# Kernel optimization log

Hardware: AMD Instinct MI355X
Metric: run time of the kernel (lower is better)

## Reference

```python
import jax, jax.numpy as jnp
import numpy as np

N_NODES = 50000
N_EDGES = 800000
D_IN = 128
D_OUT = 128


def setup_inputs() -> dict:
    key = jax.random.key(0)
    ks = jax.random.split(key, 10)
    x = jax.random.normal(ks[0], (N_NODES, D_IN), dtype=jnp.float32)
    src = jax.random.randint(ks[1], (N_EDGES,), 0, N_NODES, dtype=jnp.int32)
    dst = jax.random.randint(ks[2], (N_EDGES,), 0, N_NODES, dtype=jnp.int32)
    s = 1.0 / np.sqrt(D_IN)
    def lin(k, din, dout):
        kw, kb = jax.random.split(k)
        W = jax.random.uniform(kw, (din, dout), minval=-s, maxval=s, dtype=jnp.float32)
        b = jax.random.uniform(kb, (dout,), minval=-s, maxval=s, dtype=jnp.float32)
        return W, b
    W1, b1 = lin(ks[3], D_IN, D_IN)
    W2, b2 = lin(ks[4], D_IN, D_IN)
    W3, b3 = lin(ks[5], D_IN, D_OUT)
    return dict(x=x, W1=W1, b1=b1, W2=W2, b2=b2, W3=W3, b3=b3, src=src, dst=dst)


def reference(x, W1, b1, W2, b2, W3, b3, src, dst):
    n = x.shape[0]
    ones = jnp.ones(src.shape[0], dtype=x.dtype)
    in_deg = jax.ops.segment_sum(ones, dst, num_segments=n)    # [N]
    out_deg = jax.ops.segment_sum(ones, src, num_segments=n)   # [N]

    def sage_gcn(h, W, b):
        # DGL SAGEConv(aggregator_type='gcn'), eval mode (feat_drop = identity):
        # h_neigh = (sum_{j in N(i)} h_j + h_i) / (in_deg_i + 1); out = h_neigh @ W + b
        neigh = jax.ops.segment_sum(h[src], dst, num_segments=n)  # [N, D]
        h_neigh = (neigh + h) / (in_deg + 1.0)[:, None]
        return h_neigh @ W + b

    h = sage_gcn(x, W1, b1)
    h = sage_gcn(h, W2, b2)

    # DGL GraphConv norm='both', allow_zero_in_degree=True:
    # out = D_in^{-1/2} A D_out^{-1/2} h W + b, degrees clamped to >= 1
    norm_out = jnp.clip(out_deg, 1.0) ** -0.5
    norm_in = jnp.clip(in_deg, 1.0) ** -0.5
    hs = h * norm_out[:, None]
    agg = jax.ops.segment_sum(hs[src], dst, num_segments=n)
    out = (agg * norm_in[:, None]) @ W3 + b3
    return out
```

## Files before the change

### kernel.cpp

```cpp
#include <hip/hip_runtime.h>

#define NN 50000
#define NE 800000
#define D 128

#define CH 64
#define EPC (NE / CH)
#define RG 8
#define NPR (NN / RG)

typedef short bf16x8 __attribute__((ext_vector_type(8)));
typedef float f32x4 __attribute__((ext_vector_type(4)));


__device__ __forceinline__ unsigned bf16rne(float f) {
  unsigned u = __float_as_uint(f);
  return (u + 0x7fffu + ((u >> 16) & 1u)) >> 16;
}
__device__ __forceinline__ unsigned packbf(float lo, float hi) {
  return bf16rne(lo) | (bf16rne(hi) << 16);
}

__global__ __launch_bounds__(256) void cvtw_kernel(const float* __restrict__ x,
                                                   const float* __restrict__ W1,
                                                   const float* __restrict__ W2,
                                                   const float* __restrict__ W3,
                                                   unsigned short* __restrict__ hbf,
                                                   unsigned short* __restrict__ tbl2,
                                                   unsigned short* __restrict__ T1,
                                                   unsigned short* __restrict__ T2,
                                                   unsigned short* __restrict__ T3) {
  int b = blockIdx.x;
  int tid = threadIdx.x;
  if (b < 6250) {
    int i = b * 256 + tid;
    float4 v = ((const float4*)x)[i];
    uint2 p;
    p.x = packbf(v.x, v.y);
    p.y = packbf(v.z, v.w);
    ((uint2*)hbf)[i] = p;
  } else if (b < 6442) {
    int g = b - 6250;
    int w = g >> 6;
    int i = (g & 63) * 256 + tid;
    const float* W = (w == 0) ? W1 : (w == 1) ? W2 : W3;
    unsigned short* T = (w == 0) ? T1 : (w == 1) ? T2 : T3;
    int n = i >> 7, k = i & 127;
    T[n * 128 + k] = (unsigned short)bf16rne(W[k * 128 + n]);
  } else {
    if (tid < 16) {
      ((uint4*)(hbf + (size_t)NN * D))[tid] = make_uint4(0, 0, 0, 0);
      ((uint4*)(tbl2 + (size_t)NN * D))[tid] = make_uint4(0, 0, 0, 0);
    }
  }
}

__global__ __launch_bounds__(1024) void hist_kernel(const int* __restrict__ src,
                                                    const int* __restrict__ dst,
                                                    int* __restrict__ partial_dst,
                                                    int* __restrict__ partial_src) {
  __shared__ int hd[NPR];
  __shared__ int hs[NPR];
  int tid = threadIdx.x;
  int c = blockIdx.x >> 3;
  int r = blockIdx.x & 7;
  int base = r * NPR;
  for (int i = tid; i < NPR; i += 1024) { hd[i] = 0; hs[i] = 0; }
  __syncthreads();
  int e0 = c * EPC;
  for (int i = tid; i < EPC; i += 1024) {
    int d = dst[e0 + i];
    int s = src[e0 + i];
    unsigned dr = (unsigned)(d - base);
    unsigned sr = (unsigned)(s - base);
    if (dr < NPR) atomicAdd(&hd[dr], 1);
    if (sr < NPR) atomicAdd(&hs[sr], 1);
  }
  __syncthreads();
  for (int i = tid; i < NPR; i += 1024) {
    partial_dst[c * NN + base + i] = hd[i];
    partial_src[c * NN + base + i] = hs[i];
  }
}

__device__ __forceinline__ int block_excl_scan(int v, int* wsum) {
  int lane = threadIdx.x & 63;
  int w = threadIdx.x >> 6;
  int incl = v;
#pragma unroll
  for (int off = 1; off < 64; off <<= 1) {
    int t = __shfl_up(incl, off);
    if (lane >= off) incl += t;
  }
  if (lane == 63) wsum[w] = incl;
  __syncthreads();
  int wo = 0;
#pragma unroll
  for (int j = 0; j < 4; ++j)
    if (j < w) wo += wsum[j];
  return wo + incl - v;
}

__global__ __launch_bounds__(256) void degscan_kernel(int* __restrict__ partial_dst,
                                                      const int* __restrict__ partial_src,
                                                      int* __restrict__ degtmp,
                                                      int* __restrict__ deg_out,
                                                      int* __restrict__ row_ptr,
                                                      int* __restrict__ partials, int N) {
  __shared__ int wsum[4];
  int d = blockIdx.x * 256 + threadIdx.x;
  int run = 0;
  if (d < N) {
#pragma unroll
    for (int c = 0; c < CH; ++c) {
      int v = partial_dst[c * NN + d];
      partial_dst[c * NN + d] = run;
      run += v;
    }
    degtmp[d] = run;
    int ro = 0;
#pragma unroll
    for (int c = 0; c < CH; ++c) ro += partial_src[c * NN + d];
    deg_out[d] = ro;
  }
  int pad = (run + 15) & ~15;
  int excl = block_excl_scan(pad, wsum);
  if (d < N) row_ptr[d] = excl;
  if (threadIdx.x == 255) partials[blockIdx.x] = excl + pad;
}

__global__ __launch_bounds__(256) void scan2(int* __restrict__ partials,
                                             int* __restrict__ row_ptr, int nb, int N) {
  __shared__ int wsum[4];
  int v = (threadIdx.x < nb) ? partials[threadIdx.x] : 0;
  int excl = block_excl_scan(v, wsum);
  if (threadIdx.x < nb) partials[threadIdx.x] = excl;
  if (threadIdx.x == nb - 1) row_ptr[N] = excl + v;
}

__global__ __launch_bounds__(256) void scan3(int* __restrict__ row_ptr,
                                             const int* __restrict__ partials, int N) {
  int i = blockIdx.x * 256 + threadIdx.x;
  if (i < N) row_ptr[i] += partials[blockIdx.x];
}

__global__ __launch_bounds__(1024) void fill_kernel(const int* __restrict__ src,
                                                    const int* __restrict__ dst,
                                                    const int* __restrict__ row_ptr,
                                                    const int* __restrict__ partial_dst,
                                                    const int* __restrict__ degtmp,
                                                    int* __restrict__ csr_src) {
  __shared__ int cur[NPR];
  int tid = threadIdx.x;
  int c = blockIdx.x >> 3;
  int r = blockIdx.x & 7;
  int base = r * NPR;
  for (int i = tid; i < NPR; i += 1024)
    cur[i] = row_ptr[base + i] + partial_dst[c * NN + base + i];
  if (c == 0) {
    for (int i = tid; i < NPR; i += 1024) {
      int node = base + i;
      int s = row_ptr[node] + degtmp[node];
      int e = row_ptr[node + 1];
      for (int j = s; j < e; ++j) csr_src[j] = NN;
    }
  }
  __syncthreads();
  int e0 = c * EPC;
  for (int i = tid; i < EPC; i += 1024) {
    int d = dst[e0 + i];
    unsigned dr = (unsigned)(d - base);
    if (dr < NPR) {
      int pos = atomicAdd(&cur[dr], 1);
      csr_src[pos] = src[e0 + i];
    }
  }
}

__device__ __forceinline__ void bacc(float* a, uint4 u) {
  a[0] += __uint_as_float(u.x << 16);
  a[1] += __uint_as_float(u.x & 0xffff0000u);
  a[2] += __uint_as_float(u.y << 16);
  a[3] += __uint_as_float(u.y & 0xffff0000u);
  a[4] += __uint_as_float(u.z << 16);
  a[5] += __uint_as_float(u.z & 0xffff0000u);
  a[6] += __uint_as_float(u.w << 16);
  a[7] += __uint_as_float(u.w & 0xffff0000u);
}

template <int AMODE, int GMODE, int OUT_BF>
__global__ __launch_bounds__(256, 4) void fused_kernel(
    const unsigned short* __restrict__ hb, const int* __restrict__ row_ptr,
    const int* __restrict__ csr_src, const int* __restrict__ degtmp,
    const int* __restrict__ deg_out, const unsigned short* __restrict__ WT,
    const float* __restrict__ bias, float* __restrict__ outf,
    unsigned short* __restrict__ outb, int N) {
  __shared__ unsigned short sA[4][16 * 136];
  int tid = threadIdx.x;
  int wv = tid >> 6;
  int lane = tid & 63;
  int q = lane >> 4;
  int col = lane & 15;
  int base = blockIdx.x * 64 + wv * 16;

  for (int j = 0; j < 16; ++j) {
    int node = base + j;
    int cn = (node < N) ? node : N - 1;
    int start = row_ptr[cn];
    int iters = (row_ptr[cn + 1] - start) >> 4;
    float a0[8] = {0, 0, 0, 0, 0, 0, 0, 0};
    float a1[8] = {0, 0, 0, 0, 0, 0, 0, 0};
    float a2[8] = {0, 0, 0, 0, 0, 0, 0, 0};
    float a3[8] = {0, 0, 0, 0, 0, 0, 0, 0};
    const int* ce = csr_src + start + q;
    for (int it = 0; it < iters; ++it, ce += 16) {
      int i0 = ce[0];
      int i1 = ce[4];
      int i2 = ce[8];
      int i3 = ce[12];
      uint4 u0 = ((const uint4*)(hb + (size_t)i0 * D))[col];
      uint4 u1 = ((const uint4*)(hb + (size_t)i1 * D))[col];
      uint4 u2 = ((const uint4*)(hb + (size_t)i2 * D))[col];
      uint4 u3 = ((const uint4*)(hb + (size_t)i3 * D))[col];
      bacc(a0, u0);
      bacc(a1, u1);
      bacc(a2, u2);
      bacc(a3, u3);
    }
#pragma unroll
    for (int t = 0; t < 8; ++t) a0[t] = (a0[t] + a1[t]) + (a2[t] + a3[t]);
#pragma unroll
    for (int t = 0; t < 8; ++t) {
      a0[t] += __shfl_xor(a0[t], 16);
      a0[t] += __shfl_xor(a0[t], 32);
    }
    int indeg = degtmp[cn];
    if (AMODE == 0) {
      uint4 s = ((const uint4*)(hb + (size_t)cn * D))[col];
      float sf[8] = {0, 0, 0, 0, 0, 0, 0, 0};
      bacc(sf, s);
      float inv = 1.0f / (float)(indeg + 1);
#pragma unroll
      for (int t = 0; t < 8; ++t) a0[t] = (a0[t] + sf[t]) * inv;
    } else {
      float sc = rsqrtf(fmaxf((float)indeg, 1.0f));
#pragma unroll
      for (int t = 0; t < 8; ++t) a0[t] *= sc;
    }
    if (q == 0) {
      uint4 p;
      p.x = packbf(a0[0], a0[1]);
      p.y = packbf(a0[2], a0[3]);
      p.z = packbf(a0[4], a0[5]);
      p.w = packbf(a0[6], a0[7]);
      *(uint4*)&sA[wv][j * 136 + col * 8] = p;
    }
  }

  int ln = col;
  bf16x8 af[4];
#pragma unroll
  for (int c = 0; c < 4; ++c)
    af[c] = *(const bf16x8*)&sA[wv][ln * 136 + c * 32 + q * 8];
  f32x4 acc[8];
#pragma unroll
  for (int t = 0; t < 8; ++t) acc[t] = (f32x4){0.f, 0.f, 0.f, 0.f};
#pragma unroll
  for (int t = 0; t < 8; ++t) {
    const unsigned short* Wr = WT + (size_t)(t * 16 + ln) * 128 + q * 8;
    bf16x8 b0 = *(const bf16x8*)(Wr + 0);
    bf16x8 b1 = *(const bf16x8*)(Wr + 32);
    bf16x8 b2 = *(const bf16x8*)(Wr + 64);
    bf16x8 b3 = *(const bf16x8*)(Wr + 96);
    acc[t] = __builtin_amdgcn_mfma_f32_16x16x32_bf16(af[0], b0, acc[t], 0, 0, 0);
    acc[t] = __builtin_amdgcn_mfma_f32_16x16x32_bf16(af[1], b1, acc[t], 0, 0, 0);
    acc[t] = __builtin_amdgcn_mfma_f32_16x16x32_bf16(af[2], b2, acc[t], 0, 0, 0);
    acc[t] = __builtin_amdgcn_mfma_f32_16x16x32_bf16(af[3], b3, acc[t], 0, 0, 0);
  }
  float scl[4];
#pragma unroll
  for (int r = 0; r < 4; ++r) {
    scl[r] = 1.0f;
    if (GMODE == 1) {
      int row = base + q * 4 + r;
      int rr = (row < N) ? row : 0;
      scl[r] = rsqrtf(fmaxf((float)deg_out[rr], 1.0f));
    }
  }
#pragma unroll
  for (int t = 0; t < 8; ++t) {
    float b = bias[t * 16 + ln];
#pragma unroll
    for (int r = 0; r < 4; ++r) {
      int row = base + q * 4 + r;
      if (row < N) {
        float v = (acc[t][r] + b) * scl[r];
        if (OUT_BF)
          outb[(size_t)row * 128 + t * 16 + ln] = (unsigned short)bf16rne(v);
        else
          outf[(size_t)row * 128 + t * 16 + ln] = v;
      }
    }
  }
}


extern "C" void kernel_launch(void* const* d_in, const int* in_sizes, int n_in,
                              void* d_out, int out_size, void* d_ws, size_t ws_size,
                              hipStream_t stream) {
  const float* x = (const float*)d_in[0];
  const float* W1 = (const float*)d_in[1];
  const float* b1 = (const float*)d_in[2];
  const float* W2 = (const float*)d_in[3];
  const float* b2 = (const float*)d_in[4];
  const float* W3 = (const float*)d_in[5];
  const float* b3 = (const float*)d_in[6];
  const int* src = (const int*)d_in[7];
  const int* dst = (const int*)d_in[8];
  float* out = (float*)d_out;

  const int N = NN;

  unsigned short* hbf = (unsigned short*)d_ws;
  unsigned short* tbl2 = hbf + (size_t)(NN + 1) * D;
  unsigned short* WT1 = tbl2 + (size_t)(NN + 1) * D;
  unsigned short* WT2 = WT1 + D * D;
  unsigned short* WT3 = WT2 + D * D;
  int* partial_dst = (int*)(WT3 + D * D);
  int* partial_src = partial_dst + (size_t)CH * NN;
  int* degtmp = partial_src + (size_t)CH * NN;
  int* deg_out = degtmp + NN;
  int* row_ptr = deg_out + NN;
  int* partials = row_ptr + NN + 1;
  int* csr_src = partials + 256;

  const int scanBlocks = (N + 255) / 256;

  cvtw_kernel<<<6443, 256, 0, stream>>>(x, W1, W2, W3, hbf, tbl2, WT1, WT2, WT3);
  hist_kernel<<<CH * RG, 1024, 0, stream>>>(src, dst, partial_dst, partial_src);
  degscan_kernel<<<scanBlocks, 256, 0, stream>>>(partial_dst, partial_src, degtmp,
                                                 deg_out, row_ptr, partials, N);
  scan2<<<1, 256, 0, stream>>>(partials, row_ptr, scanBlocks, N);
  scan3<<<scanBlocks, 256, 0, stream>>>(row_ptr, partials, N);
  fill_kernel<<<CH * RG, 1024, 0, stream>>>(src, dst, row_ptr, partial_dst, degtmp, csr_src);

  int fusedBlocks = (N + 63) / 64;

  fused_kernel<0, 0, 1><<<fusedBlocks, 256, 0, stream>>>(
      hbf, row_ptr, csr_src, degtmp, deg_out, WT1, b1, nullptr, tbl2, N);
  fused_kernel<0, 1, 1><<<fusedBlocks, 256, 0, stream>>>(
      tbl2, row_ptr, csr_src, degtmp, deg_out, WT2, b2, nullptr, hbf, N);
  fused_kernel<1, 0, 0><<<fusedBlocks, 256, 0, stream>>>(
      hbf, row_ptr, csr_src, degtmp, deg_out, WT3, b3, out, nullptr, N);
}
```

Measured before the change: 317.0 us.

## Shrink fused blocks to 16 nodes and split MFMA output columns across waves

Each block now handles 16 nodes instead of 64. Each wave aggregates 4 nodes into one shared tile, then after a block barrier computes 2 of the 8 output column tiles. This gives 4x more blocks, which should help load balance across CUs for the irregular gather. It also cuts the per-wave MFMA accumulator count, and the N bounds checks are dropped on the assumption that N is a multiple of 16. The cost is an added __syncthreads and removal of the min-blocks-per-CU launch bound hint.

```diff
diff --git a/kernel.cpp b/kernel.cpp
--- a/kernel.cpp
+++ b/kernel.cpp
@@ -189,25 +189,26 @@
 }
 
 template <int AMODE, int GMODE, int OUT_BF>
-__global__ __launch_bounds__(256, 4) void fused_kernel(
+__global__ __launch_bounds__(256) void fused_kernel(
     const unsigned short* __restrict__ hb, const int* __restrict__ row_ptr,
     const int* __restrict__ csr_src, const int* __restrict__ degtmp,
     const int* __restrict__ deg_out, const unsigned short* __restrict__ WT,
     const float* __restrict__ bias, float* __restrict__ outf,
     unsigned short* __restrict__ outb, int N) {
-  __shared__ unsigned short sA[4][16 * 136];
+  __shared__ unsigned short sA[16 * 136];
   int tid = threadIdx.x;
   int wv = tid >> 6;
   int lane = tid & 63;
   int q = lane >> 4;
   int col = lane & 15;
-  int base = blockIdx.x * 64 + wv * 16;
-
-  for (int j = 0; j < 16; ++j) {
-    int node = base + j;
-    int cn = (node < N) ? node : N - 1;
-    int start = row_ptr[cn];
-    int iters = (row_ptr[cn + 1] - start) >> 4;
+  int base = blockIdx.x * 16;
+
+#pragma unroll
+  for (int j = 0; j < 4; ++j) {
+    int jt = wv * 4 + j;
+    int node = base + jt;
+    int start = row_ptr[node];
+    int iters = (row_ptr[node + 1] - start) >> 4;
     float a0[8] = {0, 0, 0, 0, 0, 0, 0, 0};
     float a1[8] = {0, 0, 0, 0, 0, 0, 0, 0};
     float a2[8] = {0, 0, 0, 0, 0, 0, 0, 0};
@@ -234,9 +235,9 @@
       a0[t] += __shfl_xor(a0[t], 16);
       a0[t] += __shfl_xor(a0[t], 32);
     }
-    int indeg = degtmp[cn];
+    int indeg = degtmp[node];
     if (AMODE == 0) {
-      uint4 s = ((const uint4*)(hb + (size_t)cn * D))[col];
+      uint4 s = ((const uint4*)(hb + (size_t)node * D))[col];
       float sf[8] = {0, 0, 0, 0, 0, 0, 0, 0};
       bacc(sf, s);
       float inv = 1.0f / (float)(indeg + 1);
@@ -253,21 +254,23 @@
       p.y = packbf(a0[2], a0[3]);
       p.z = packbf(a0[4], a0[5]);
       p.w = packbf(a0[6], a0[7]);
-      *(uint4*)&sA[wv][j * 136 + col * 8] = p;
-    }
-  }
+      *(uint4*)&sA[jt * 136 + col * 8] = p;
+    }
+  }
+  __syncthreads();
 
   int ln = col;
   bf16x8 af[4];
 #pragma unroll
   for (int c = 0; c < 4; ++c)
-    af[c] = *(const bf16x8*)&sA[wv][ln * 136 + c * 32 + q * 8];
-  f32x4 acc[8];
-#pragma unroll
-  for (int t = 0; t < 8; ++t) acc[t] = (f32x4){0.f, 0.f, 0.f, 0.f};
-#pragma unroll
-  for (int t = 0; t < 8; ++t) {
-    const unsigned short* Wr = WT + (size_t)(t * 16 + ln) * 128 + q * 8;
+    af[c] = *(const bf16x8*)&sA[ln * 136 + c * 32 + q * 8];
+  f32x4 acc[2];
+#pragma unroll
+  for (int t = 0; t < 2; ++t) acc[t] = (f32x4){0.f, 0.f, 0.f, 0.f};
+#pragma unroll
+  for (int t = 0; t < 2; ++t) {
+    int nt = wv * 2 + t;
+    const unsigned short* Wr = WT + (size_t)(nt * 16 + ln) * 128 + q * 8;
     bf16x8 b0 = *(const bf16x8*)(Wr + 0);
     bf16x8 b1 = *(const bf16x8*)(Wr + 32);
     bf16x8 b2 = *(const bf16x8*)(Wr + 64);
@@ -281,25 +284,20 @@
 #pragma unroll
   for (int r = 0; r < 4; ++r) {
     scl[r] = 1.0f;
-    if (GMODE == 1) {
-      int row = base + q * 4 + r;
-      int rr = (row < N) ? row : 0;
-      scl[r] = rsqrtf(fmaxf((float)deg_out[rr], 1.0f));
-    }
-  }
-#pragma unroll
-  for (int t = 0; t < 8; ++t) {
-    float b = bias[t * 16 + ln];
+    if (GMODE == 1) scl[r] = rsqrtf(fmaxf((float)deg_out[base + q * 4 + r], 1.0f));
+  }
+#pragma unroll
+  for (int t = 0; t < 2; ++t) {
+    int nt = wv * 2 + t;
+    float b = bias[nt * 16 + ln];
 #pragma unroll
     for (int r = 0; r < 4; ++r) {
       int row = base + q * 4 + r;
-      if (row < N) {
-        float v = (acc[t][r] + b) * scl[r];
-        if (OUT_BF)
-          outb[(size_t)row * 128 + t * 16 + ln] = (unsigned short)bf16rne(v);
-        else
-          outf[(size_t)row * 128 + t * 16 + ln] = v;
-      }
+      float v = (acc[t][r] + b) * scl[r];
+      if (OUT_BF)
+        outb[(size_t)row * 128 + nt * 16 + ln] = (unsigned short)bf16rne(v);
+      else
+        outf[(size_t)row * 128 + nt * 16 + ln] = v;
     }
   }
 }
@@ -344,7 +342,7 @@
   scan3<<<scanBlocks, 256, 0, stream>>>(row_ptr, partials, N);
   fill_kernel<<<CH * RG, 1024, 0, stream>>>(src, dst, row_ptr, partial_dst, degtmp, csr_src);
 
-  int fusedBlocks = (N + 63) / 64;
+  int fusedBlocks = N / 16;
 
   fused_kernel<0, 0, 1><<<fusedBlocks, 256, 0, stream>>>(
       hbf, row_ptr, csr_src, degtmp, deg_out, WT1, b1, nullptr, tbl2, N);
```

New measurement: 284.6 us. 10.2% less time.
